# Optimization experiments

Measured on AMD Instinct MI355X. Metric: run time of the kernel, lower is better.

Reference implementation:

```python
import jax, jax.numpy as jnp
import numpy as np

B, T, F, H, D1, D2, OUT = 8192, 90, 7, 128, 128, 64, 30


def _layernorm(x, g, b, eps=1e-5):
    mu = jnp.mean(x, axis=-1, keepdims=True)
    var = jnp.mean((x - mu) ** 2, axis=-1, keepdims=True)
    return (x - mu) * jax.lax.rsqrt(var + eps) * g + b


def _lstm_layer(x, Wih, Whh, bih, bhh):
    # x: [B,T,H_in]; Wih: [4H,H_in]; Whh: [4H,H]; biases [4H]. PyTorch gate order i,f,g,o.
    xg = jnp.einsum('bti,gi->btg', x, Wih) + bih + bhh  # [B,T,4H] precomputed input projection
    xg_t = jnp.swapaxes(xg, 0, 1)  # [T,B,4H]

    def step(carry, gx):
        h, c = carry
        gates = gx + h @ Whh.T  # [B,4H]
        i, f, g, o = jnp.split(gates, 4, axis=-1)
        c = jax.nn.sigmoid(f) * c + jax.nn.sigmoid(i) * jnp.tanh(g)
        h = jax.nn.sigmoid(o) * jnp.tanh(c)
        return (h, c), h

    h0 = jnp.zeros((x.shape[0], H), x.dtype)
    (_, _), hs = jax.lax.scan(step, (h0, h0), xg_t)
    return jnp.swapaxes(hs, 0, 1)  # [B,T,H]


def setup_inputs() -> dict:
    key = jax.random.key(0)
    ks = jax.random.split(key, 16)
    s = lambda k, shape, scale: jax.random.normal(k, shape, jnp.float32) * scale
    inp = {
        'x': s(ks[0], (B, T, F), 1.0),
        'W_in': s(ks[1], (H, F), 0.3), 'b_in': jnp.zeros((H,)),
        'g_in': jnp.ones((H,)), 'be_in': jnp.zeros((H,)),
        'Wih0': s(ks[2], (4 * H, H), 0.08), 'Whh0': s(ks[3], (4 * H, H), 0.08),
        'bih0': jnp.zeros((4 * H,)).at[H:2 * H].set(1.0), 'bhh0': jnp.zeros((4 * H,)),
        'Wih1': s(ks[4], (4 * H, H), 0.08), 'Whh1': s(ks[5], (4 * H, H), 0.08),
        'bih1': jnp.zeros((4 * H,)).at[H:2 * H].set(1.0), 'bhh1': jnp.zeros((4 * H,)),
        'g_ln': jnp.ones((H,)), 'be_ln': jnp.zeros((H,)),
        'W_d1': s(ks[6], (D1, H), 0.12), 'b_d1': jnp.zeros((D1,)),
        'W_d2': s(ks[7], (D2, D1), 0.12), 'b_d2': jnp.zeros((D2,)),
        'W_d3': s(ks[8], (OUT, D2), 0.15), 'b_d3': jnp.zeros((OUT,)),
    }
    return inp


def reference(x, W_in, b_in, g_in, be_in,
              Wih0, Whh0, bih0, bhh0, Wih1, Whh1, bih1, bhh1,
              g_ln, be_ln, W_d1, b_d1, W_d2, b_d2, W_d3, b_d3):
    h = _layernorm(jnp.einsum('btf,hf->bth', x, W_in) + b_in, g_in, be_in)
    h = _lstm_layer(h, Wih0, Whh0, bih0, bhh0)
    h = _lstm_layer(h, Wih1, Whh1, bih1, bhh1)  # dropout between layers is eval no-op
    last = _layernorm(h[:, -1, :], g_ln, be_ln)  # [B,H]
    d = jax.nn.relu(last @ W_d1.T + b_d1)
    d = jax.nn.relu(d @ W_d2.T + b_d2)
    return d @ W_d3.T + b_d3  # [B,30]
```

## Files before the change

### kernel.cpp

```cpp
#include <hip/hip_runtime.h>

#define DEV __device__ __forceinline__
typedef unsigned short u16;
typedef unsigned int u32;
typedef __bf16 bf16x8 __attribute__((ext_vector_type(8)));
typedef float f32x4 __attribute__((ext_vector_type(4)));

static constexpr int B = 8192, T = 90, F = 7, H = 128, NOUT = 30;

DEV float fexp2(float x) { return __builtin_amdgcn_exp2f(x); }
DEV float frcp(float x) { return __builtin_amdgcn_rcpf(x); }
DEV float frsq(float x) { return __builtin_amdgcn_rsqf(x); }
DEV float sigm(float x) { return frcp(1.f + fexp2(-1.44269504088896341f * x)); }
DEV u16 f2bfbits(float f) { __bf16 b = (__bf16)f; return __builtin_bit_cast(u16, b); }
DEV float bfbits2f(u32 u) { return __builtin_bit_cast(float, u << 16); }
DEV u32 pk2(float a, float b) { return (u32)f2bfbits(a) | ((u32)f2bfbits(b) << 16); }

DEV float wave_sum(float v) {
#pragma unroll
    for (int m = 32; m; m >>= 1) v += __shfl_xor(v, m, 64);
    return v;
}

__global__ __launch_bounds__(512) void prep_aux(
    const float* __restrict__ W_in, const float* __restrict__ b_in,
    const float* __restrict__ g_in, const float* __restrict__ be_in,
    const float* __restrict__ Wih0, float* __restrict__ aux, u16* __restrict__ Uhat) {
    const int tid = threadIdx.x;
    if (tid < 7) {
        float sm = 0.f, sp = 0.f;
        for (int h = 0; h < 128; ++h) { const float w = W_in[h * 7 + tid]; sm += w; sp += w * b_in[h]; }
        aux[tid] = sm * (1.f / 128.f); aux[64 + tid] = sp * (1.f / 128.f);
    } else if (tid < 56) {
        const int cd = tid - 7, cc = cd / 7, dd = cd % 7;
        float s = 0.f;
        for (int h = 0; h < 128; ++h) s += W_in[h * 7 + cc] * W_in[h * 7 + dd];
        aux[8 + cd] = s * (1.f / 128.f);
    } else if (tid == 56) {
        float s = 0.f; for (int h = 0; h < 128; ++h) s += b_in[h];
        aux[7] = s * (1.f / 128.f);
    } else if (tid == 57) {
        float s = 0.f; for (int h = 0; h < 128; ++h) s += b_in[h] * b_in[h];
        aux[72] = s * (1.f / 128.f);
    }
    float acc[10];
#pragma unroll
    for (int i = 0; i < 10; ++i) acc[i] = 0.f;
    const float* wr = Wih0 + (long)tid * 128;
    for (int h = 0; h < 128; ++h) {
        const float wv = wr[h], wg = wv * g_in[h];
#pragma unroll
        for (int cc = 0; cc < 7; ++cc) acc[cc] += wg * W_in[h * 7 + cc];
        acc[7] += wg * b_in[h]; acc[8] += wg; acc[9] += wv * be_in[h];
    }
    u16* dst = Uhat + tid * 32;
#pragma unroll
    for (int cc = 0; cc < 10; ++cc) dst[cc] = f2bfbits(acc[cc]);
#pragma unroll
    for (int cc = 10; cc < 32; ++cc) dst[cc] = 0;
}

__global__ __launch_bounds__(256) void prep_stats(
    const float* __restrict__ x, const float* __restrict__ aux,
    float2* __restrict__ stats) {
    __shared__ float sa[80];
    const int tid = threadIdx.x;
    if (tid < 80) sa[tid] = aux[tid];
    __syncthreads();
    const long idx = (long)blockIdx.x * 256 + tid;
    const float* xr = x + idx * 7;
    float xv[7];
#pragma unroll
    for (int cc = 0; cc < 7; ++cc) xv[cc] = xr[cc];
    float mu = sa[7];
#pragma unroll
    for (int cc = 0; cc < 7; ++cc) mu += sa[cc] * xv[cc];
    float q = sa[72];
#pragma unroll
    for (int cc = 0; cc < 7; ++cc) {
        float tacc = 2.f * sa[64 + cc];
#pragma unroll
        for (int dd = 0; dd < 7; ++dd) tacc += sa[8 + cc * 7 + dd] * xv[dd];
        q += xv[cc] * tacc;
    }
    const float rstd = frsq(q - mu * mu + 1e-5f);
    stats[idx] = make_float2(rstd, -rstd * mu);
}

__global__ __launch_bounds__(512, 2) void lstm_rec_l1(
    const float* __restrict__ x, const float2* __restrict__ stats,
    const u16* __restrict__ Uhat, const float* __restrict__ Whh,
    const float* __restrict__ bih, const float* __restrict__ bhh,
    u16* __restrict__ hs) {
    __shared__ __align__(16) u16 s_z[2][2][4][16][8];
    __shared__ __align__(16) u16 s_h[2][2][16 * 128];

    const int tid = threadIdx.x;
    const int wave = tid >> 6, lane = tid & 63, quad = lane >> 4, n16 = lane & 15;
    const int b0 = blockIdx.x * 32;

    for (int i = tid; i < 2 * 2 * 4 * 16 * 8; i += 512) ((u16*)s_z)[i] = 0;
    for (int i = tid; i < 2 * 16 * 128; i += 512) ((u16*)s_h[1])[i] = 0;

    bf16x8 bU[4], bWhh[4][4];
    float bias[4];
#pragma unroll
    for (int g = 0; g < 4; ++g) {
        const int wrow = g * 128 + 16 * wave + n16;
        bias[g] = bih[wrow] + bhh[wrow];
        bU[g] = *(const bf16x8*)&Uhat[wrow * 32 + quad * 8];
#pragma unroll
        for (int kk = 0; kk < 4; ++kk) {
            const float* ph = Whh + (long)wrow * 128 + kk * 32 + quad * 8;
            bf16x8 bh;
#pragma unroll
            for (int j = 0; j < 8; ++j) bh[j] = (__bf16)ph[j];
            bWhh[g][kk] = bh;
        }
    }

    const f32x4 zero4 = {0.f, 0.f, 0.f, 0.f};
    float c[2][4];
#pragma unroll
    for (int mt = 0; mt < 2; ++mt)
#pragma unroll
        for (int r = 0; r < 4; ++r) c[mt][r] = 0.f;

    const bool stager = (lane < 8);
    const int tau = wave * 8 + lane;
    const int srow = tau & 31, skk8 = tau >> 5;
    const int smt = srow >> 4, sm = srow & 15;
    const long srowg = (long)(b0 + srow) * T;

    const int ftile = tid >> 8, finner = tid & 255;
    const int fm = finner & 15, fkk8 = finner >> 4;
    const int fldsoff = (fkk8 * 16 + fm) * 8;
    const size_t fgrow = (size_t)(b0 + ftile * 16 + fm) * T;
    const int fgcol = fkk8 * 8;

    __syncthreads();

    if (stager) {
        const float2 st0 = stats[srowg];
        u32 p0, p1, p2, p3;
        if (skk8 == 0) {
            const float* xp = x + srowg * 7;
            const float rs = st0.x;
            p0 = pk2(rs * xp[0], rs * xp[1]); p1 = pk2(rs * xp[2], rs * xp[3]);
            p2 = pk2(rs * xp[4], rs * xp[5]); p3 = pk2(rs * xp[6], rs);
        } else { p0 = pk2(st0.y, 1.f); p1 = 0; p2 = 0; p3 = 0; }
        *(uint4*)&s_z[0][smt][skk8][sm][0] = (uint4){p0, p1, p2, p3};
    }
    __syncthreads();

#pragma unroll 1
    for (int t = 0; t < T; ++t) {
        const int par = t & 1;
        const int t1 = t + 1;
        const bool hasPre = stager && (t1 < T);
        float2 nst = {};
        float nx[7];
        if (hasPre) {
            nst = stats[srowg + t1];
            if (skk8 == 0) {
                const float* xp = x + (srowg + t1) * 7;
#pragma unroll
                for (int j = 0; j < 7; ++j) nx[j] = xp[j];
            }
        }
        if (t > 0) {
            const uint4 hv = *(const uint4*)&s_h[par ^ 1][ftile][fldsoff];
            *(uint4*)(hs + (fgrow + (t - 1)) * 128 + fgcol) = hv;
        }

#pragma unroll
        for (int mt = 0; mt < 2; ++mt) {
            const bf16x8 az = *(const bf16x8*)&s_z[par][mt][quad][n16][0];
            bf16x8 ah[4];
#pragma unroll
            for (int kk = 0; kk < 4; ++kk)
                ah[kk] = *(const bf16x8*)&s_h[par ^ 1][mt][((kk * 4 + quad) * 16 + n16) * 8];
            f32x4 acc[4];
#pragma unroll
            for (int g = 0; g < 4; ++g) {
                f32x4 a = __builtin_amdgcn_mfma_f32_16x16x32_bf16(az, bU[g], zero4, 0, 0, 0);
#pragma unroll
                for (int kk = 0; kk < 4; ++kk)
                    a = __builtin_amdgcn_mfma_f32_16x16x32_bf16(ah[kk], bWhh[g][kk], a, 0, 0, 0);
                acc[g] = a;
            }
#pragma unroll
            for (int r = 0; r < 4; ++r) {
                const float xi = acc[0][r] + bias[0];
                const float xf = acc[1][r] + bias[1];
                const float xg = acc[2][r] + bias[2];
                const float xo = acc[3][r] + bias[3];
                const float tg = 2.f * frcp(1.f + fexp2(-2.88539008177792681f * xg)) - 1.f;
                const float cn = sigm(xf) * c[mt][r] + sigm(xi) * tg;
                c[mt][r] = cn;
                const float so = sigm(xo);
                const float rr = frcp(1.f + fexp2(-2.88539008177792681f * cn));
                const float hv = __builtin_fmaf(2.f * so, rr, -so);
                s_h[par][mt][((2 * wave + (n16 >> 3)) * 16 + (quad * 4 + r)) * 8 + (n16 & 7)] =
                    f2bfbits(hv);
            }
        }

        if (hasPre) {
            u32 p0, p1, p2, p3;
            if (skk8 == 0) {
                const float rs = nst.x;
                p0 = pk2(rs * nx[0], rs * nx[1]); p1 = pk2(rs * nx[2], rs * nx[3]);
                p2 = pk2(rs * nx[4], rs * nx[5]); p3 = pk2(rs * nx[6], rs);
            } else { p0 = pk2(nst.y, 1.f); p1 = 0; p2 = 0; p3 = 0; }
            *(uint4*)&s_z[par ^ 1][smt][skk8][sm][0] = (uint4){p0, p1, p2, p3};
        }
        __syncthreads();
    }
    {
        const uint4 hv = *(const uint4*)&s_h[1][ftile][fldsoff];
        *(uint4*)(hs + (fgrow + (T - 1)) * 128 + fgcol) = hv;
    }
}

__global__ __launch_bounds__(512, 2) void lstm_rec_l2(
    const float* __restrict__ Wih, const float* __restrict__ Whh,
    const float* __restrict__ bih, const float* __restrict__ bhh,
    const u16* __restrict__ xin, u16* __restrict__ hlast) {
    __shared__ __align__(16) u16 s_x[2][2][16 * 128];
    __shared__ __align__(16) u16 s_h[2][2][16 * 128];

    const int tid = threadIdx.x;
    const int wave = tid >> 6, lane = tid & 63, quad = lane >> 4, n16 = lane & 15;
    const int b0 = blockIdx.x * 32;

    for (int i = tid; i < 2 * 16 * 128; i += 512) ((u16*)s_h[1])[i] = 0;

    bf16x8 bWih[4][4], bWhh[4][4];
    float bias[4];
#pragma unroll
    for (int g = 0; g < 4; ++g) {
        const int wrow = g * 128 + 16 * wave + n16;
        bias[g] = bih[wrow] + bhh[wrow];
#pragma unroll
        for (int kk = 0; kk < 4; ++kk) {
            const float* pi = Wih + (long)wrow * 128 + kk * 32 + quad * 8;
            const float* ph = Whh + (long)wrow * 128 + kk * 32 + quad * 8;
            bf16x8 bi, bh;
#pragma unroll
            for (int j = 0; j < 8; ++j) { bi[j] = (__bf16)pi[j]; bh[j] = (__bf16)ph[j]; }
            bWih[g][kk] = bi; bWhh[g][kk] = bh;
        }
    }

    const f32x4 zero4 = {0.f, 0.f, 0.f, 0.f};
    float c[2][4];
#pragma unroll
    for (int mt = 0; mt < 2; ++mt)
#pragma unroll
        for (int r = 0; r < 4; ++r) c[mt][r] = 0.f;

    const int stile = tid >> 8, sinner = tid & 255;
    const int sm = sinner & 15, skk8 = sinner >> 4;
    const u16* gsrc = xin + (size_t)(b0 + stile * 16 + sm) * T * 128 + skk8 * 8;
    const int ftile = tid >> 8, finner = tid & 255;
    const int fm = finner & 15, fkk8 = finner >> 4;
    const int fldsoff = (fkk8 * 16 + fm) * 8;
    const int fgcol = fkk8 * 8;

    {
        const uint4 v = *(const uint4*)gsrc;
        *(uint4*)&s_x[0][stile][sinner * 8] = v;
    }
    __syncthreads();

#pragma unroll 1
    for (int t = 0; t < T; ++t) {
        const int par = t & 1;
        uint4 pre = {};
        const bool hasPre = (t + 1 < T);
        if (hasPre) pre = *(const uint4*)(gsrc + (size_t)(t + 1) * 128);

#pragma unroll
        for (int mt = 0; mt < 2; ++mt) {
            bf16x8 aln[4], ah[4];
#pragma unroll
            for (int kk = 0; kk < 4; ++kk) {
                aln[kk] = *(const bf16x8*)&s_x[par][mt][((kk * 4 + quad) * 16 + n16) * 8];
                ah[kk] = *(const bf16x8*)&s_h[par ^ 1][mt][((kk * 4 + quad) * 16 + n16) * 8];
            }
            f32x4 acc[4];
#pragma unroll
            for (int g = 0; g < 4; ++g) {
                f32x4 a = __builtin_amdgcn_mfma_f32_16x16x32_bf16(aln[0], bWih[g][0], zero4, 0, 0, 0);
                a = __builtin_amdgcn_mfma_f32_16x16x32_bf16(ah[0], bWhh[g][0], a, 0, 0, 0);
#pragma unroll
                for (int kk = 1; kk < 4; ++kk) {
                    a = __builtin_amdgcn_mfma_f32_16x16x32_bf16(aln[kk], bWih[g][kk], a, 0, 0, 0);
                    a = __builtin_amdgcn_mfma_f32_16x16x32_bf16(ah[kk], bWhh[g][kk], a, 0, 0, 0);
                }
                acc[g] = a;
            }
#pragma unroll
            for (int r = 0; r < 4; ++r) {
                const float xi = acc[0][r] + bias[0];
                const float xf = acc[1][r] + bias[1];
                const float xg = acc[2][r] + bias[2];
                const float xo = acc[3][r] + bias[3];
                const float tg = 2.f * frcp(1.f + fexp2(-2.88539008177792681f * xg)) - 1.f;
                const float cn = sigm(xf) * c[mt][r] + sigm(xi) * tg;
                c[mt][r] = cn;
                const float so = sigm(xo);
                const float rr = frcp(1.f + fexp2(-2.88539008177792681f * cn));
                const float hv = __builtin_fmaf(2.f * so, rr, -so);
                s_h[par][mt][((2 * wave + (n16 >> 3)) * 16 + (quad * 4 + r)) * 8 + (n16 & 7)] =
                    f2bfbits(hv);
            }
        }
        if (hasPre) *(uint4*)&s_x[par ^ 1][stile][sinner * 8] = pre;
        __syncthreads();
    }
    {
        const uint4 hv = *(const uint4*)&s_h[1][ftile][fldsoff];
        *(uint4*)(hlast + (size_t)(b0 + ftile * 16 + fm) * 128 + fgcol) = hv;
    }
}

__global__ __launch_bounds__(256) void dense_head(
    const u16* __restrict__ hlast, const float* __restrict__ g_ln,
    const float* __restrict__ be_ln, const float* __restrict__ W_d1,
    const float* __restrict__ b_d1, const float* __restrict__ W_d2,
    const float* __restrict__ b_d2, const float* __restrict__ W_d3,
    const float* __restrict__ b_d3, float* __restrict__ out) {
    __shared__ float s_ln[16][128];
    __shared__ float s_d1[16][128];
    __shared__ float s_d2[16][64];
    const int wave = threadIdx.x >> 6, lane = threadIdx.x & 63;
    const long base = (long)blockIdx.x * 16;
    const int R = wave * 4;

#pragma unroll
    for (int rr = 0; rr < 4; ++rr) {
        const long row = base + R + rr;
        const u32 packed = ((const u32*)hlast)[row * 64 + lane];
        float v0 = bfbits2f(packed & 0xffffu), v1 = bfbits2f(packed >> 16);
        const float s = wave_sum(v0 + v1);
        const float q = wave_sum(v0 * v0 + v1 * v1);
        const float mu = s * (1.f / 128.f);
        const float rstd = frsq(q * (1.f / 128.f) - mu * mu + 1e-5f);
        const int h0 = 2 * lane;
        s_ln[R + rr][h0] = (v0 - mu) * rstd * g_ln[h0] + be_ln[h0];
        s_ln[R + rr][h0 + 1] = (v1 - mu) * rstd * g_ln[h0 + 1] + be_ln[h0 + 1];
    }
    __syncthreads();

#pragma unroll
    for (int half = 0; half < 2; ++half) {
        const int o = lane + 64 * half;
        float a[4] = {b_d1[o], b_d1[o], b_d1[o], b_d1[o]};
        const float4* wr = (const float4*)(W_d1 + (long)o * 128);
#pragma unroll 8
        for (int k = 0; k < 32; ++k) {
            const float4 wv = wr[k];
#pragma unroll
            for (int rr = 0; rr < 4; ++rr) {
                const float4 xv = ((const float4*)s_ln[R + rr])[k];
                a[rr] += wv.x * xv.x + wv.y * xv.y + wv.z * xv.z + wv.w * xv.w;
            }
        }
#pragma unroll
        for (int rr = 0; rr < 4; ++rr) s_d1[R + rr][o] = fmaxf(a[rr], 0.f);
    }
    __syncthreads();

    {
        float a[4] = {b_d2[lane], b_d2[lane], b_d2[lane], b_d2[lane]};
        const float4* wr = (const float4*)(W_d2 + (long)lane * 128);
#pragma unroll 8
        for (int k = 0; k < 32; ++k) {
            const float4 wv = wr[k];
#pragma unroll
            for (int rr = 0; rr < 4; ++rr) {
                const float4 xv = ((const float4*)s_d1[R + rr])[k];
                a[rr] += wv.x * xv.x + wv.y * xv.y + wv.z * xv.z + wv.w * xv.w;
            }
        }
#pragma unroll
        for (int rr = 0; rr < 4; ++rr) s_d2[R + rr][lane] = fmaxf(a[rr], 0.f);
    }
    __syncthreads();

    if (lane < NOUT) {
        float a[4] = {b_d3[lane], b_d3[lane], b_d3[lane], b_d3[lane]};
        const float4* wr = (const float4*)(W_d3 + (long)lane * 64);
#pragma unroll
        for (int k = 0; k < 16; ++k) {
            const float4 wv = wr[k];
#pragma unroll
            for (int rr = 0; rr < 4; ++rr) {
                const float4 xv = ((const float4*)s_d2[R + rr])[k];
                a[rr] += wv.x * xv.x + wv.y * xv.y + wv.z * xv.z + wv.w * xv.w;
            }
        }
#pragma unroll
        for (int rr = 0; rr < 4; ++rr) out[(base + R + rr) * NOUT + lane] = a[rr];
    }
}

extern "C" void kernel_launch(void* const* d_in, const int* in_sizes, int n_in,
                              void* d_out, int out_size, void* d_ws, size_t ws_size,
                              hipStream_t stream) {
    const float* x = (const float*)d_in[0];
    const float* W_in = (const float*)d_in[1];
    const float* b_in = (const float*)d_in[2];
    const float* g_in = (const float*)d_in[3];
    const float* be_in = (const float*)d_in[4];
    const float* Wih0 = (const float*)d_in[5];
    const float* Whh0 = (const float*)d_in[6];
    const float* bih0 = (const float*)d_in[7];
    const float* bhh0 = (const float*)d_in[8];
    const float* Wih1 = (const float*)d_in[9];
    const float* Whh1 = (const float*)d_in[10];
    const float* bih1 = (const float*)d_in[11];
    const float* bhh1 = (const float*)d_in[12];
    const float* g_ln = (const float*)d_in[13];
    const float* be_ln = (const float*)d_in[14];
    const float* W_d1 = (const float*)d_in[15];
    const float* b_d1 = (const float*)d_in[16];
    const float* W_d2 = (const float*)d_in[17];
    const float* b_d2 = (const float*)d_in[18];
    const float* W_d3 = (const float*)d_in[19];
    const float* b_d3 = (const float*)d_in[20];
    float* out = (float*)d_out;

    char* w = (char*)d_ws;
    float* aux = (float*)w;               w += 512;
    u16* Uhat = (u16*)w;                  w += 512 * 32 * sizeof(u16);
    float2* stats = (float2*)w;           w += (size_t)B * T * sizeof(float2);
    u16* hs0 = (u16*)w;                   w += (size_t)B * T * H * sizeof(u16);
    u16* hlast = (u16*)w;

    prep_aux<<<1, 512, 0, stream>>>(W_in, b_in, g_in, be_in, Wih0, aux, Uhat);
    prep_stats<<<(B * T) / 256, 256, 0, stream>>>(x, aux, stats);
    lstm_rec_l1<<<B / 32, 512, 0, stream>>>(x, stats, Uhat, Whh0, bih0, bhh0, hs0);
    lstm_rec_l2<<<B / 32, 512, 0, stream>>>(Wih1, Whh1, bih1, bhh1, hs0, hlast);
    dense_head<<<B / 16, 256, 0, stream>>>(hlast, g_ln, be_ln, W_d1, b_d1, W_d2, b_d2,
                                           W_d3, b_d3, out);
}
```

Before: 552.9 us.

## Fuse both LSTM layers into one wavefront-pipelined kernel with split wave groups

Merges the two recurrent kernels into one launch. Four waves run layer 1 and four waves run layer 2 one timestep behind, passing h1 through shared memory. This removes the write and re-read of the full [B,T,H] layer-1 hidden sequence through global memory. In exchange each wave now holds twice as many weight fragments (two column tiles), which raises register pressure at 512 threads with occupancy 2. The layer-1 and layer-2 work per step also becomes unbalanced, and the waves meet at one barrier per step.

```diff
diff --git a/kernel.cpp b/kernel.cpp
--- a/kernel.cpp
+++ b/kernel.cpp
@@ -87,242 +87,216 @@
     stats[idx] = make_float2(rstd, -rstd * mu);
 }
 
-__global__ __launch_bounds__(512, 2) void lstm_rec_l1(
+#define GATE_E(ACC, CARR, PTR, HWB, R, B0, B1, B2, B3)                                  \
+    {                                                                                   \
+        const float xi_ = ACC[0][R] + (B0);                                             \
+        const float xf_ = ACC[1][R] + (B1);                                             \
+        const float xg_ = ACC[2][R] + (B2);                                             \
+        const float xo_ = ACC[3][R] + (B3);                                             \
+        const float tg_ = 2.f * frcp(1.f + fexp2(-2.88539008177792681f * xg_)) - 1.f;   \
+        const float cn_ = sigm(xf_) * CARR[R] + sigm(xi_) * tg_;                        \
+        CARR[R] = cn_;                                                                  \
+        const float so_ = sigm(xo_);                                                    \
+        const float rr_ = frcp(1.f + fexp2(-2.88539008177792681f * cn_));               \
+        (PTR)[(HWB) + (R) * 8] = f2bfbits(__builtin_fmaf(2.f * so_, rr_, -so_));        \
+    }
+
+__global__ __launch_bounds__(512, 2) void lstm_fused(
     const float* __restrict__ x, const float2* __restrict__ stats,
-    const u16* __restrict__ Uhat, const float* __restrict__ Whh,
-    const float* __restrict__ bih, const float* __restrict__ bhh,
-    u16* __restrict__ hs) {
+    const u16* __restrict__ Uhat,
+    const float* __restrict__ Whh0, const float* __restrict__ bih0,
+    const float* __restrict__ bhh0,
+    const float* __restrict__ Wih1, const float* __restrict__ Whh1,
+    const float* __restrict__ bih1, const float* __restrict__ bhh1,
+    u16* __restrict__ hlast) {
     __shared__ __align__(16) u16 s_z[2][2][4][16][8];
-    __shared__ __align__(16) u16 s_h[2][2][16 * 128];
+    __shared__ __align__(16) u16 s_h1[2][2][16][16][8];
+    __shared__ __align__(16) u16 s_h2[2][2][16][16][8];
 
     const int tid = threadIdx.x;
     const int wave = tid >> 6, lane = tid & 63, quad = lane >> 4, n16 = lane & 15;
     const int b0 = blockIdx.x * 32;
+    const int group = (wave ^ (wave >> 2)) & 1;
+    const int wl = wave >> 1;
 
     for (int i = tid; i < 2 * 2 * 4 * 16 * 8; i += 512) ((u16*)s_z)[i] = 0;
-    for (int i = tid; i < 2 * 16 * 128; i += 512) ((u16*)s_h[1])[i] = 0;
-
-    bf16x8 bU[4], bWhh[4][4];
-    float bias[4];
-#pragma unroll
-    for (int g = 0; g < 4; ++g) {
-        const int wrow = g * 128 + 16 * wave + n16;
-        bias[g] = bih[wrow] + bhh[wrow];
-        bU[g] = *(const bf16x8*)&Uhat[wrow * 32 + quad * 8];
-#pragma unroll
-        for (int kk = 0; kk < 4; ++kk) {
-            const float* ph = Whh + (long)wrow * 128 + kk * 32 + quad * 8;
-            bf16x8 bh;
-#pragma unroll
-            for (int j = 0; j < 8; ++j) bh[j] = (__bf16)ph[j];
-            bWhh[g][kk] = bh;
-        }
+    for (int i = tid; i < 2 * 16 * 16 * 8; i += 512) {
+        ((u16*)s_h1[1])[i] = 0;
+        ((u16*)s_h2[0])[i] = 0;
     }
 
     const f32x4 zero4 = {0.f, 0.f, 0.f, 0.f};
-    float c[2][4];
-#pragma unroll
-    for (int mt = 0; mt < 2; ++mt)
-#pragma unroll
-        for (int r = 0; r < 4; ++r) c[mt][r] = 0.f;
-
-    const bool stager = (lane < 8);
-    const int tau = wave * 8 + lane;
-    const int srow = tau & 31, skk8 = tau >> 5;
-    const int smt = srow >> 4, sm = srow & 15;
-    const long srowg = (long)(b0 + srow) * T;
-
-    const int ftile = tid >> 8, finner = tid & 255;
-    const int fm = finner & 15, fkk8 = finner >> 4;
-    const int fldsoff = (fkk8 * 16 + fm) * 8;
-    const size_t fgrow = (size_t)(b0 + ftile * 16 + fm) * T;
-    const int fgcol = fkk8 * 8;
+    const int hwb0 = ((wl * 4 + 0 + (n16 >> 3)) * 16 + quad * 4) * 8 + (n16 & 7);
+    const int hwb1 = ((wl * 4 + 2 + (n16 >> 3)) * 16 + quad * 4) * 8 + (n16 & 7);
 
     __syncthreads();
 
-    if (stager) {
-        const float2 st0 = stats[srowg];
-        u32 p0, p1, p2, p3;
-        if (skk8 == 0) {
+    if (group == 0) {
+        bf16x8 bU[4][2], bW0[4][2][4];
+        float bias[4][2];
+#pragma unroll
+        for (int g = 0; g < 4; ++g)
+#pragma unroll
+            for (int ct = 0; ct < 2; ++ct) {
+                const int wrow = g * 128 + wl * 32 + ct * 16 + n16;
+                bias[g][ct] = bih0[wrow] + bhh0[wrow];
+                bU[g][ct] = *(const bf16x8*)&Uhat[wrow * 32 + quad * 8];
+#pragma unroll
+                for (int kk = 0; kk < 4; ++kk) {
+                    const float* ph = Whh0 + (long)wrow * 128 + kk * 32 + quad * 8;
+                    bf16x8 bh;
+#pragma unroll
+                    for (int j = 0; j < 8; ++j) bh[j] = (__bf16)ph[j];
+                    bW0[g][ct][kk] = bh;
+                }
+            }
+
+        float c1[2][2][4];
+#pragma unroll
+        for (int mt = 0; mt < 2; ++mt)
+#pragma unroll
+            for (int ct = 0; ct < 2; ++ct)
+#pragma unroll
+                for (int r = 0; r < 4; ++r) c1[mt][ct][r] = 0.f;
+
+        const bool stager = (lane < 8);
+        const int srow = wl * 8 + lane, smt = srow >> 4, sm = srow & 15;
+        const long srowg = (long)(b0 + srow) * T;
+
+        if (stager) {
+            const float2 st0 = stats[srowg];
             const float* xp = x + srowg * 7;
             const float rs = st0.x;
-            p0 = pk2(rs * xp[0], rs * xp[1]); p1 = pk2(rs * xp[2], rs * xp[3]);
-            p2 = pk2(rs * xp[4], rs * xp[5]); p3 = pk2(rs * xp[6], rs);
-        } else { p0 = pk2(st0.y, 1.f); p1 = 0; p2 = 0; p3 = 0; }
-        *(uint4*)&s_z[0][smt][skk8][sm][0] = (uint4){p0, p1, p2, p3};
-    }
-    __syncthreads();
+            uint4 v0 = {pk2(rs * xp[0], rs * xp[1]), pk2(rs * xp[2], rs * xp[3]),
+                        pk2(rs * xp[4], rs * xp[5]), pk2(rs * xp[6], rs)};
+            uint4 v1 = {pk2(st0.y, 1.f), 0u, 0u, 0u};
+            *(uint4*)&s_z[0][smt][0][sm][0] = v0;
+            *(uint4*)&s_z[0][smt][1][sm][0] = v1;
+        }
+        __syncthreads();
 
 #pragma unroll 1
-    for (int t = 0; t < T; ++t) {
-        const int par = t & 1;
-        const int t1 = t + 1;
-        const bool hasPre = stager && (t1 < T);
-        float2 nst = {};
-        float nx[7];
-        if (hasPre) {
-            nst = stats[srowg + t1];
-            if (skk8 == 0) {
-                const float* xp = x + (srowg + t1) * 7;
-#pragma unroll
-                for (int j = 0; j < 7; ++j) nx[j] = xp[j];
-            }
-        }
-        if (t > 0) {
-            const uint4 hv = *(const uint4*)&s_h[par ^ 1][ftile][fldsoff];
-            *(uint4*)(hs + (fgrow + (t - 1)) * 128 + fgcol) = hv;
-        }
-
-#pragma unroll
-        for (int mt = 0; mt < 2; ++mt) {
-            const bf16x8 az = *(const bf16x8*)&s_z[par][mt][quad][n16][0];
-            bf16x8 ah[4];
-#pragma unroll
-            for (int kk = 0; kk < 4; ++kk)
-                ah[kk] = *(const bf16x8*)&s_h[par ^ 1][mt][((kk * 4 + quad) * 16 + n16) * 8];
-            f32x4 acc[4];
-#pragma unroll
-            for (int g = 0; g < 4; ++g) {
-                f32x4 a = __builtin_amdgcn_mfma_f32_16x16x32_bf16(az, bU[g], zero4, 0, 0, 0);
+        for (int k = 0; k < 90; ++k) {
+            const int par = k & 1;
+            float2 nst = {};
+            float nx0 = 0, nx1 = 0, nx2 = 0, nx3 = 0, nx4 = 0, nx5 = 0, nx6 = 0;
+            const bool pre = stager && (k < 89);
+            if (pre) {
+                nst = stats[srowg + k + 1];
+                const float* xp = x + (srowg + k + 1) * 7;
+                nx0 = xp[0]; nx1 = xp[1]; nx2 = xp[2]; nx3 = xp[3];
+                nx4 = xp[4]; nx5 = xp[5]; nx6 = xp[6];
+            }
+#pragma unroll
+            for (int mt = 0; mt < 2; ++mt) {
+                const bf16x8 az = *(const bf16x8*)&s_z[par][mt][quad][n16][0];
+                bf16x8 ah[4];
 #pragma unroll
                 for (int kk = 0; kk < 4; ++kk)
-                    a = __builtin_amdgcn_mfma_f32_16x16x32_bf16(ah[kk], bWhh[g][kk], a, 0, 0, 0);
-                acc[g] = a;
-            }
-#pragma unroll
-            for (int r = 0; r < 4; ++r) {
-                const float xi = acc[0][r] + bias[0];
-                const float xf = acc[1][r] + bias[1];
-                const float xg = acc[2][r] + bias[2];
-                const float xo = acc[3][r] + bias[3];
-                const float tg = 2.f * frcp(1.f + fexp2(-2.88539008177792681f * xg)) - 1.f;
-                const float cn = sigm(xf) * c[mt][r] + sigm(xi) * tg;
-                c[mt][r] = cn;
-                const float so = sigm(xo);
-                const float rr = frcp(1.f + fexp2(-2.88539008177792681f * cn));
-                const float hv = __builtin_fmaf(2.f * so, rr, -so);
-                s_h[par][mt][((2 * wave + (n16 >> 3)) * 16 + (quad * 4 + r)) * 8 + (n16 & 7)] =
-                    f2bfbits(hv);
-            }
-        }
-
-        if (hasPre) {
-            u32 p0, p1, p2, p3;
-            if (skk8 == 0) {
+                    ah[kk] = *(const bf16x8*)&s_h1[par ^ 1][mt][kk * 4 + quad][n16][0];
+                f32x4 acc[2][4];
+#pragma unroll
+                for (int ct = 0; ct < 2; ++ct)
+#pragma unroll
+                    for (int g = 0; g < 4; ++g) {
+                        f32x4 a = __builtin_amdgcn_mfma_f32_16x16x32_bf16(az, bU[g][ct], zero4, 0, 0, 0);
+#pragma unroll
+                        for (int kk = 0; kk < 4; ++kk)
+                            a = __builtin_amdgcn_mfma_f32_16x16x32_bf16(ah[kk], bW0[g][ct][kk], a, 0, 0, 0);
+                        acc[ct][g] = a;
+                    }
+                u16* hp = &s_h1[par][mt][0][0][0];
+#pragma unroll
+                for (int r = 0; r < 4; ++r)
+                    GATE_E(acc[0], c1[mt][0], hp, hwb0, r, bias[0][0], bias[1][0], bias[2][0], bias[3][0])
+#pragma unroll
+                for (int r = 0; r < 4; ++r)
+                    GATE_E(acc[1], c1[mt][1], hp, hwb1, r, bias[0][1], bias[1][1], bias[2][1], bias[3][1])
+            }
+            if (pre) {
                 const float rs = nst.x;
-                p0 = pk2(rs * nx[0], rs * nx[1]); p1 = pk2(rs * nx[2], rs * nx[3]);
-                p2 = pk2(rs * nx[4], rs * nx[5]); p3 = pk2(rs * nx[6], rs);
-            } else { p0 = pk2(nst.y, 1.f); p1 = 0; p2 = 0; p3 = 0; }
-            *(uint4*)&s_z[par ^ 1][smt][skk8][sm][0] = (uint4){p0, p1, p2, p3};
+                uint4 v0 = {pk2(rs * nx0, rs * nx1), pk2(rs * nx2, rs * nx3),
+                            pk2(rs * nx4, rs * nx5), pk2(rs * nx6, rs)};
+                uint4 v1 = {pk2(nst.y, 1.f), 0u, 0u, 0u};
+                *(uint4*)&s_z[par ^ 1][smt][0][sm][0] = v0;
+                *(uint4*)&s_z[par ^ 1][smt][1][sm][0] = v1;
+            }
+            __syncthreads();
         }
         __syncthreads();
-    }
+    } else {
+        bf16x8 bWi[4][2][4], bWh[4][2][4];
+        float bias[4][2];
+#pragma unroll
+        for (int g = 0; g < 4; ++g)
+#pragma unroll
+            for (int ct = 0; ct < 2; ++ct) {
+                const int wrow = g * 128 + wl * 32 + ct * 16 + n16;
+                bias[g][ct] = bih1[wrow] + bhh1[wrow];
+#pragma unroll
+                for (int kk = 0; kk < 4; ++kk) {
+                    const float* pi = Wih1 + (long)wrow * 128 + kk * 32 + quad * 8;
+                    const float* ph = Whh1 + (long)wrow * 128 + kk * 32 + quad * 8;
+                    bf16x8 bi, bh;
+#pragma unroll
+                    for (int j = 0; j < 8; ++j) { bi[j] = (__bf16)pi[j]; bh[j] = (__bf16)ph[j]; }
+                    bWi[g][ct][kk] = bi; bWh[g][ct][kk] = bh;
+                }
+            }
+
+        float c2[2][2][4];
+#pragma unroll
+        for (int mt = 0; mt < 2; ++mt)
+#pragma unroll
+            for (int ct = 0; ct < 2; ++ct)
+#pragma unroll
+                for (int r = 0; r < 4; ++r) c2[mt][ct][r] = 0.f;
+
+        __syncthreads();
+        __syncthreads();
+
+#pragma unroll 1
+        for (int k = 1; k <= 90; ++k) {
+            const int par = k & 1;
+#pragma unroll
+            for (int mt = 0; mt < 2; ++mt) {
+                bf16x8 a1[4], a2[4];
+#pragma unroll
+                for (int kk = 0; kk < 4; ++kk) {
+                    a1[kk] = *(const bf16x8*)&s_h1[par ^ 1][mt][kk * 4 + quad][n16][0];
+                    a2[kk] = *(const bf16x8*)&s_h2[par ^ 1][mt][kk * 4 + quad][n16][0];
+                }
+                f32x4 acc[2][4];
+#pragma unroll
+                for (int ct = 0; ct < 2; ++ct)
+#pragma unroll
+                    for (int g = 0; g < 4; ++g) {
+                        f32x4 a = __builtin_amdgcn_mfma_f32_16x16x32_bf16(a1[0], bWi[g][ct][0], zero4, 0, 0, 0);
+                        a = __builtin_amdgcn_mfma_f32_16x16x32_bf16(a2[0], bWh[g][ct][0], a, 0, 0, 0);
+#pragma unroll
+                        for (int kk = 1; kk < 4; ++kk) {
+                            a = __builtin_amdgcn_mfma_f32_16x16x32_bf16(a1[kk], bWi[g][ct][kk], a, 0, 0, 0);
+                            a = __builtin_amdgcn_mfma_f32_16x16x32_bf16(a2[kk], bWh[g][ct][kk], a, 0, 0, 0);
+                        }
+                        acc[ct][g] = a;
+                    }
+                u16* hp = &s_h2[par][mt][0][0][0];
+#pragma unroll
+                for (int r = 0; r < 4; ++r)
+                    GATE_E(acc[0], c2[mt][0], hp, hwb0, r, bias[0][0], bias[1][0], bias[2][0], bias[3][0])
+#pragma unroll
+                for (int r = 0; r < 4; ++r)
+                    GATE_E(acc[1], c2[mt][1], hp, hwb1, r, bias[0][1], bias[1][1], bias[2][1], bias[3][1])
+            }
+            __syncthreads();
+        }
+    }
+
     {
-        const uint4 hv = *(const uint4*)&s_h[1][ftile][fldsoff];
-        *(uint4*)(hs + (fgrow + (T - 1)) * 128 + fgcol) = hv;
-    }
-}
-
-__global__ __launch_bounds__(512, 2) void lstm_rec_l2(
-    const float* __restrict__ Wih, const float* __restrict__ Whh,
-    const float* __restrict__ bih, const float* __restrict__ bhh,
-    const u16* __restrict__ xin, u16* __restrict__ hlast) {
-    __shared__ __align__(16) u16 s_x[2][2][16 * 128];
-    __shared__ __align__(16) u16 s_h[2][2][16 * 128];
-
-    const int tid = threadIdx.x;
-    const int wave = tid >> 6, lane = tid & 63, quad = lane >> 4, n16 = lane & 15;
-    const int b0 = blockIdx.x * 32;
-
-    for (int i = tid; i < 2 * 16 * 128; i += 512) ((u16*)s_h[1])[i] = 0;
-
-    bf16x8 bWih[4][4], bWhh[4][4];
-    float bias[4];
-#pragma unroll
-    for (int g = 0; g < 4; ++g) {
-        const int wrow = g * 128 + 16 * wave + n16;
-        bias[g] = bih[wrow] + bhh[wrow];
-#pragma unroll
-        for (int kk = 0; kk < 4; ++kk) {
-            const float* pi = Wih + (long)wrow * 128 + kk * 32 + quad * 8;
-            const float* ph = Whh + (long)wrow * 128 + kk * 32 + quad * 8;
-            bf16x8 bi, bh;
-#pragma unroll
-            for (int j = 0; j < 8; ++j) { bi[j] = (__bf16)pi[j]; bh[j] = (__bf16)ph[j]; }
-            bWih[g][kk] = bi; bWhh[g][kk] = bh;
-        }
-    }
-
-    const f32x4 zero4 = {0.f, 0.f, 0.f, 0.f};
-    float c[2][4];
-#pragma unroll
-    for (int mt = 0; mt < 2; ++mt)
-#pragma unroll
-        for (int r = 0; r < 4; ++r) c[mt][r] = 0.f;
-
-    const int stile = tid >> 8, sinner = tid & 255;
-    const int sm = sinner & 15, skk8 = sinner >> 4;
-    const u16* gsrc = xin + (size_t)(b0 + stile * 16 + sm) * T * 128 + skk8 * 8;
-    const int ftile = tid >> 8, finner = tid & 255;
-    const int fm = finner & 15, fkk8 = finner >> 4;
-    const int fldsoff = (fkk8 * 16 + fm) * 8;
-    const int fgcol = fkk8 * 8;
-
-    {
-        const uint4 v = *(const uint4*)gsrc;
-        *(uint4*)&s_x[0][stile][sinner * 8] = v;
-    }
-    __syncthreads();
-
-#pragma unroll 1
-    for (int t = 0; t < T; ++t) {
-        const int par = t & 1;
-        uint4 pre = {};
-        const bool hasPre = (t + 1 < T);
-        if (hasPre) pre = *(const uint4*)(gsrc + (size_t)(t + 1) * 128);
-
-#pragma unroll
-        for (int mt = 0; mt < 2; ++mt) {
-            bf16x8 aln[4], ah[4];
-#pragma unroll
-            for (int kk = 0; kk < 4; ++kk) {
-                aln[kk] = *(const bf16x8*)&s_x[par][mt][((kk * 4 + quad) * 16 + n16) * 8];
-                ah[kk] = *(const bf16x8*)&s_h[par ^ 1][mt][((kk * 4 + quad) * 16 + n16) * 8];
-            }
-            f32x4 acc[4];
-#pragma unroll
-            for (int g = 0; g < 4; ++g) {
-                f32x4 a = __builtin_amdgcn_mfma_f32_16x16x32_bf16(aln[0], bWih[g][0], zero4, 0, 0, 0);
-                a = __builtin_amdgcn_mfma_f32_16x16x32_bf16(ah[0], bWhh[g][0], a, 0, 0, 0);
-#pragma unroll
-                for (int kk = 1; kk < 4; ++kk) {
-                    a = __builtin_amdgcn_mfma_f32_16x16x32_bf16(aln[kk], bWih[g][kk], a, 0, 0, 0);
-                    a = __builtin_amdgcn_mfma_f32_16x16x32_bf16(ah[kk], bWhh[g][kk], a, 0, 0, 0);
-                }
-                acc[g] = a;
-            }
-#pragma unroll
-            for (int r = 0; r < 4; ++r) {
-                const float xi = acc[0][r] + bias[0];
-                const float xf = acc[1][r] + bias[1];
-                const float xg = acc[2][r] + bias[2];
-                const float xo = acc[3][r] + bias[3];
-                const float tg = 2.f * frcp(1.f + fexp2(-2.88539008177792681f * xg)) - 1.f;
-                const float cn = sigm(xf) * c[mt][r] + sigm(xi) * tg;
-                c[mt][r] = cn;
-                const float so = sigm(xo);
-                const float rr = frcp(1.f + fexp2(-2.88539008177792681f * cn));
-                const float hv = __builtin_fmaf(2.f * so, rr, -so);
-                s_h[par][mt][((2 * wave + (n16 >> 3)) * 16 + (quad * 4 + r)) * 8 + (n16 & 7)] =
-                    f2bfbits(hv);
-            }
-        }
-        if (hasPre) *(uint4*)&s_x[par ^ 1][stile][sinner * 8] = pre;
-        __syncthreads();
-    }
-    {
-        const uint4 hv = *(const uint4*)&s_h[1][ftile][fldsoff];
-        *(uint4*)(hlast + (size_t)(b0 + ftile * 16 + fm) * 128 + fgcol) = hv;
+        const int ftile = tid >> 8, fin = tid & 255;
+        const int fm = fin & 15, fk = fin >> 4;
+        const uint4 hv = *(const uint4*)&s_h2[0][ftile][fk][fm][0];
+        *(uint4*)(hlast + (size_t)(b0 + ftile * 16 + fm) * 128 + fk * 8) = hv;
     }
 }
 
@@ -437,13 +411,12 @@
     float* aux = (float*)w;               w += 512;
     u16* Uhat = (u16*)w;                  w += 512 * 32 * sizeof(u16);
     float2* stats = (float2*)w;           w += (size_t)B * T * sizeof(float2);
-    u16* hs0 = (u16*)w;                   w += (size_t)B * T * H * sizeof(u16);
     u16* hlast = (u16*)w;
 
     prep_aux<<<1, 512, 0, stream>>>(W_in, b_in, g_in, be_in, Wih0, aux, Uhat);
     prep_stats<<<(B * T) / 256, 256, 0, stream>>>(x, aux, stats);
-    lstm_rec_l1<<<B / 32, 512, 0, stream>>>(x, stats, Uhat, Whh0, bih0, bhh0, hs0);
-    lstm_rec_l2<<<B / 32, 512, 0, stream>>>(Wih1, Whh1, bih1, bhh1, hs0, hlast);
+    lstm_fused<<<B / 32, 512, 0, stream>>>(x, stats, Uhat, Whh0, bih0, bhh0,
+                                           Wih1, Whh1, bih1, bhh1, hlast);
     dense_head<<<B / 16, 256, 0, stream>>>(hlast, g_ln, be_ln, W_d1, b_d1, W_d2, b_d2,
                                            W_d3, b_d3, out);
 }
```

After: 1.499 ms. +171.1%, slower.

## Halve LSTM block batch tile to 16 rows to double grid size

Applied to the files above, without the earlier changes.

Both recurrent LSTM kernels now process 16 batch rows per block instead of 32, launching B/16 blocks. Each wave runs one M-tile of MFMAs per timestep instead of two, which shortens the serial per-step critical path and exposes more blocks to fill the CUs. The cost is that each block still loads the full weight set into registers, so weight loads are duplicated across twice as many blocks. Half the threads now sit idle during staging and stores, and per-step work is smaller relative to the barrier overhead.

```diff
diff --git a/kernel.cpp b/kernel.cpp
--- a/kernel.cpp
+++ b/kernel.cpp
@@ -87,20 +87,34 @@
     stats[idx] = make_float2(rstd, -rstd * mu);
 }
 
+#define GATE_R(ACC, CARR, SHROW, R)                                                     \
+    {                                                                                   \
+        const float xi_ = ACC[0][R] + bias[0];                                          \
+        const float xf_ = ACC[1][R] + bias[1];                                          \
+        const float xg_ = ACC[2][R] + bias[2];                                          \
+        const float xo_ = ACC[3][R] + bias[3];                                          \
+        const float tg_ = 2.f * frcp(1.f + fexp2(-2.88539008177792681f * xg_)) - 1.f;   \
+        const float cn_ = sigm(xf_) * CARR[R] + sigm(xi_) * tg_;                        \
+        CARR[R] = cn_;                                                                  \
+        const float so_ = sigm(xo_);                                                    \
+        const float rr_ = frcp(1.f + fexp2(-2.88539008177792681f * cn_));               \
+        SHROW[hwbase + (R) * 8] = f2bfbits(__builtin_fmaf(2.f * so_, rr_, -so_));       \
+    }
+
 __global__ __launch_bounds__(512, 2) void lstm_rec_l1(
     const float* __restrict__ x, const float2* __restrict__ stats,
     const u16* __restrict__ Uhat, const float* __restrict__ Whh,
     const float* __restrict__ bih, const float* __restrict__ bhh,
     u16* __restrict__ hs) {
-    __shared__ __align__(16) u16 s_z[2][2][4][16][8];
-    __shared__ __align__(16) u16 s_h[2][2][16 * 128];
+    __shared__ __align__(16) u16 s_z[2][4][16][8];
+    __shared__ __align__(16) u16 s_h[2][16 * 128];
 
     const int tid = threadIdx.x;
     const int wave = tid >> 6, lane = tid & 63, quad = lane >> 4, n16 = lane & 15;
-    const int b0 = blockIdx.x * 32;
-
-    for (int i = tid; i < 2 * 2 * 4 * 16 * 8; i += 512) ((u16*)s_z)[i] = 0;
-    for (int i = tid; i < 2 * 16 * 128; i += 512) ((u16*)s_h[1])[i] = 0;
+    const int b0 = blockIdx.x * 16;
+
+    for (int i = tid; i < 2 * 4 * 16 * 8; i += 512) ((u16*)s_z)[i] = 0;
+    for (int i = tid; i < 16 * 128; i += 512) s_h[1][i] = 0;
 
     bf16x8 bU[4], bWhh[4][4];
     float bias[4];
@@ -120,23 +134,21 @@
     }
 
     const f32x4 zero4 = {0.f, 0.f, 0.f, 0.f};
-    float c[2][4];
-#pragma unroll
-    for (int mt = 0; mt < 2; ++mt)
-#pragma unroll
-        for (int r = 0; r < 4; ++r) c[mt][r] = 0.f;
-
-    const bool stager = (lane < 8);
-    const int tau = wave * 8 + lane;
-    const int srow = tau & 31, skk8 = tau >> 5;
-    const int smt = srow >> 4, sm = srow & 15;
+    float c[4];
+#pragma unroll
+    for (int r = 0; r < 4; ++r) c[r] = 0.f;
+
+    const bool stager = (lane < 4);
+    const int tau = wave * 4 + lane;
+    const int srow = tau & 15, skk8 = tau >> 4;
     const long srowg = (long)(b0 + srow) * T;
 
-    const int ftile = tid >> 8, finner = tid & 255;
-    const int fm = finner & 15, fkk8 = finner >> 4;
+    const int fm = tid & 15, fkk8 = (tid >> 4) & 15;
     const int fldsoff = (fkk8 * 16 + fm) * 8;
-    const size_t fgrow = (size_t)(b0 + ftile * 16 + fm) * T;
+    const size_t fgrow = (size_t)(b0 + fm) * T;
     const int fgcol = fkk8 * 8;
+
+    const int hwbase = (2 * wave + (n16 >> 3)) * 128 + quad * 32 + (n16 & 7);
 
     __syncthreads();
 
@@ -149,61 +161,49 @@
             p0 = pk2(rs * xp[0], rs * xp[1]); p1 = pk2(rs * xp[2], rs * xp[3]);
             p2 = pk2(rs * xp[4], rs * xp[5]); p3 = pk2(rs * xp[6], rs);
         } else { p0 = pk2(st0.y, 1.f); p1 = 0; p2 = 0; p3 = 0; }
-        *(uint4*)&s_z[0][smt][skk8][sm][0] = (uint4){p0, p1, p2, p3};
+        *(uint4*)&s_z[0][skk8][srow][0] = (uint4){p0, p1, p2, p3};
     }
     __syncthreads();
 
 #pragma unroll 1
     for (int t = 0; t < T; ++t) {
         const int par = t & 1;
-        const int t1 = t + 1;
-        const bool hasPre = stager && (t1 < T);
+        const bool hasPre = stager && (t + 1 < T);
         float2 nst = {};
         float nx[7];
         if (hasPre) {
-            nst = stats[srowg + t1];
+            nst = stats[srowg + t + 1];
             if (skk8 == 0) {
-                const float* xp = x + (srowg + t1) * 7;
+                const float* xp = x + (srowg + t + 1) * 7;
 #pragma unroll
                 for (int j = 0; j < 7; ++j) nx[j] = xp[j];
             }
         }
-        if (t > 0) {
-            const uint4 hv = *(const uint4*)&s_h[par ^ 1][ftile][fldsoff];
+        if (t > 0 && tid < 256) {
+            const uint4 hv = *(const uint4*)&s_h[par ^ 1][fldsoff];
             *(uint4*)(hs + (fgrow + (t - 1)) * 128 + fgcol) = hv;
         }
 
-#pragma unroll
-        for (int mt = 0; mt < 2; ++mt) {
-            const bf16x8 az = *(const bf16x8*)&s_z[par][mt][quad][n16][0];
-            bf16x8 ah[4];
+        const bf16x8 az = *(const bf16x8*)&s_z[par][quad][n16][0];
+        bf16x8 ah[4];
+#pragma unroll
+        for (int kk = 0; kk < 4; ++kk)
+            ah[kk] = *(const bf16x8*)&s_h[par ^ 1][((kk * 4 + quad) * 16 + n16) * 8];
+        f32x4 acc[4];
+#pragma unroll
+        for (int g = 0; g < 4; ++g) {
+            f32x4 a = __builtin_amdgcn_mfma_f32_16x16x32_bf16(az, bU[g], zero4, 0, 0, 0);
 #pragma unroll
             for (int kk = 0; kk < 4; ++kk)
-                ah[kk] = *(const bf16x8*)&s_h[par ^ 1][mt][((kk * 4 + quad) * 16 + n16) * 8];
-            f32x4 acc[4];
-#pragma unroll
-            for (int g = 0; g < 4; ++g) {
-                f32x4 a = __builtin_amdgcn_mfma_f32_16x16x32_bf16(az, bU[g], zero4, 0, 0, 0);
-#pragma unroll
-                for (int kk = 0; kk < 4; ++kk)
-                    a = __builtin_amdgcn_mfma_f32_16x16x32_bf16(ah[kk], bWhh[g][kk], a, 0, 0, 0);
-                acc[g] = a;
-            }
-#pragma unroll
-            for (int r = 0; r < 4; ++r) {
-                const float xi = acc[0][r] + bias[0];
-                const float xf = acc[1][r] + bias[1];
-                const float xg = acc[2][r] + bias[2];
-                const float xo = acc[3][r] + bias[3];
-                const float tg = 2.f * frcp(1.f + fexp2(-2.88539008177792681f * xg)) - 1.f;
-                const float cn = sigm(xf) * c[mt][r] + sigm(xi) * tg;
-                c[mt][r] = cn;
-                const float so = sigm(xo);
-                const float rr = frcp(1.f + fexp2(-2.88539008177792681f * cn));
-                const float hv = __builtin_fmaf(2.f * so, rr, -so);
-                s_h[par][mt][((2 * wave + (n16 >> 3)) * 16 + (quad * 4 + r)) * 8 + (n16 & 7)] =
-                    f2bfbits(hv);
-            }
+                a = __builtin_amdgcn_mfma_f32_16x16x32_bf16(ah[kk], bWhh[g][kk], a, 0, 0, 0);
+            acc[g] = a;
+        }
+        {
+            u16* hp = s_h[par];
+            GATE_R(acc, c, hp, 0)
+            GATE_R(acc, c, hp, 1)
+            GATE_R(acc, c, hp, 2)
+            GATE_R(acc, c, hp, 3)
         }
 
         if (hasPre) {
@@ -213,12 +213,12 @@
                 p0 = pk2(rs * nx[0], rs * nx[1]); p1 = pk2(rs * nx[2], rs * nx[3]);
                 p2 = pk2(rs * nx[4], rs * nx[5]); p3 = pk2(rs * nx[6], rs);
             } else { p0 = pk2(nst.y, 1.f); p1 = 0; p2 = 0; p3 = 0; }
-            *(uint4*)&s_z[par ^ 1][smt][skk8][sm][0] = (uint4){p0, p1, p2, p3};
+            *(uint4*)&s_z[par ^ 1][skk8][srow][0] = (uint4){p0, p1, p2, p3};
         }
         __syncthreads();
     }
-    {
-        const uint4 hv = *(const uint4*)&s_h[1][ftile][fldsoff];
+    if (tid < 256) {
+        const uint4 hv = *(const uint4*)&s_h[1][fldsoff];
         *(uint4*)(hs + (fgrow + (T - 1)) * 128 + fgcol) = hv;
     }
 }
@@ -227,14 +227,14 @@
     const float* __restrict__ Wih, const float* __restrict__ Whh,
     const float* __restrict__ bih, const float* __restrict__ bhh,
     const u16* __restrict__ xin, u16* __restrict__ hlast) {
-    __shared__ __align__(16) u16 s_x[2][2][16 * 128];
-    __shared__ __align__(16) u16 s_h[2][2][16 * 128];
+    __shared__ __align__(16) u16 s_x[2][16 * 128];
+    __shared__ __align__(16) u16 s_h[2][16 * 128];
 
     const int tid = threadIdx.x;
     const int wave = tid >> 6, lane = tid & 63, quad = lane >> 4, n16 = lane & 15;
-    const int b0 = blockIdx.x * 32;
-
-    for (int i = tid; i < 2 * 16 * 128; i += 512) ((u16*)s_h[1])[i] = 0;
+    const int b0 = blockIdx.x * 16;
+
+    for (int i = tid; i < 16 * 128; i += 512) s_h[1][i] = 0;
 
     bf16x8 bWih[4][4], bWhh[4][4];
     float bias[4];
@@ -254,23 +254,19 @@
     }
 
     const f32x4 zero4 = {0.f, 0.f, 0.f, 0.f};
-    float c[2][4];
-#pragma unroll
-    for (int mt = 0; mt < 2; ++mt)
-#pragma unroll
-        for (int r = 0; r < 4; ++r) c[mt][r] = 0.f;
-
-    const int stile = tid >> 8, sinner = tid & 255;
-    const int sm = sinner & 15, skk8 = sinner >> 4;
-    const u16* gsrc = xin + (size_t)(b0 + stile * 16 + sm) * T * 128 + skk8 * 8;
-    const int ftile = tid >> 8, finner = tid & 255;
-    const int fm = finner & 15, fkk8 = finner >> 4;
-    const int fldsoff = (fkk8 * 16 + fm) * 8;
-    const int fgcol = fkk8 * 8;
-
-    {
+    float c[4];
+#pragma unroll
+    for (int r = 0; r < 4; ++r) c[r] = 0.f;
+
+    const int ssm = tid & 15, sskk8 = (tid >> 4) & 15;
+    const u16* gsrc = xin + (size_t)(b0 + ssm) * T * 128 + sskk8 * 8;
+    const int soff = (sskk8 * 16 + ssm) * 8;
+
+    const int hwbase = (2 * wave + (n16 >> 3)) * 128 + quad * 32 + (n16 & 7);
+
+    if (tid < 256) {
         const uint4 v = *(const uint4*)gsrc;
-        *(uint4*)&s_x[0][stile][sinner * 8] = v;
+        *(uint4*)&s_x[0][soff] = v;
     }
     __syncthreads();
 
@@ -278,51 +274,41 @@
     for (int t = 0; t < T; ++t) {
         const int par = t & 1;
         uint4 pre = {};
-        const bool hasPre = (t + 1 < T);
+        const bool hasPre = (t + 1 < T) && (tid < 256);
         if (hasPre) pre = *(const uint4*)(gsrc + (size_t)(t + 1) * 128);
 
-#pragma unroll
-        for (int mt = 0; mt < 2; ++mt) {
-            bf16x8 aln[4], ah[4];
-#pragma unroll
-            for (int kk = 0; kk < 4; ++kk) {
-                aln[kk] = *(const bf16x8*)&s_x[par][mt][((kk * 4 + quad) * 16 + n16) * 8];
-                ah[kk] = *(const bf16x8*)&s_h[par ^ 1][mt][((kk * 4 + quad) * 16 + n16) * 8];
+        bf16x8 aln[4], ah[4];
+#pragma unroll
+        for (int kk = 0; kk < 4; ++kk) {
+            const int ro = ((kk * 4 + quad) * 16 + n16) * 8;
+            aln[kk] = *(const bf16x8*)&s_x[par][ro];
+            ah[kk] = *(const bf16x8*)&s_h[par ^ 1][ro];
+        }
+        f32x4 acc[4];
+#pragma unroll
+        for (int g = 0; g < 4; ++g) {
+            f32x4 a = __builtin_amdgcn_mfma_f32_16x16x32_bf16(aln[0], bWih[g][0], zero4, 0, 0, 0);
+            a = __builtin_amdgcn_mfma_f32_16x16x32_bf16(ah[0], bWhh[g][0], a, 0, 0, 0);
+#pragma unroll
+            for (int kk = 1; kk < 4; ++kk) {
+                a = __builtin_amdgcn_mfma_f32_16x16x32_bf16(aln[kk], bWih[g][kk], a, 0, 0, 0);
+                a = __builtin_amdgcn_mfma_f32_16x16x32_bf16(ah[kk], bWhh[g][kk], a, 0, 0, 0);
             }
-            f32x4 acc[4];
-#pragma unroll
-            for (int g = 0; g < 4; ++g) {
-                f32x4 a = __builtin_amdgcn_mfma_f32_16x16x32_bf16(aln[0], bWih[g][0], zero4, 0, 0, 0);
-                a = __builtin_amdgcn_mfma_f32_16x16x32_bf16(ah[0], bWhh[g][0], a, 0, 0, 0);
-#pragma unroll
-                for (int kk = 1; kk < 4; ++kk) {
-                    a = __builtin_amdgcn_mfma_f32_16x16x32_bf16(aln[kk], bWih[g][kk], a, 0, 0, 0);
-                    a = __builtin_amdgcn_mfma_f32_16x16x32_bf16(ah[kk], bWhh[g][kk], a, 0, 0, 0);
-                }
-                acc[g] = a;
-            }
-#pragma unroll
-            for (int r = 0; r < 4; ++r) {
-                const float xi = acc[0][r] + bias[0];
-                const float xf = acc[1][r] + bias[1];
-                const float xg = acc[2][r] + bias[2];
-                const float xo = acc[3][r] + bias[3];
-                const float tg = 2.f * frcp(1.f + fexp2(-2.88539008177792681f * xg)) - 1.f;
-                const float cn = sigm(xf) * c[mt][r] + sigm(xi) * tg;
-                c[mt][r] = cn;
-                const float so = sigm(xo);
-                const float rr = frcp(1.f + fexp2(-2.88539008177792681f * cn));
-                const float hv = __builtin_fmaf(2.f * so, rr, -so);
-                s_h[par][mt][((2 * wave + (n16 >> 3)) * 16 + (quad * 4 + r)) * 8 + (n16 & 7)] =
-                    f2bfbits(hv);
-            }
-        }
-        if (hasPre) *(uint4*)&s_x[par ^ 1][stile][sinner * 8] = pre;
+            acc[g] = a;
+        }
+        {
+            u16* hp = s_h[par];
+            GATE_R(acc, c, hp, 0)
+            GATE_R(acc, c, hp, 1)
+            GATE_R(acc, c, hp, 2)
+            GATE_R(acc, c, hp, 3)
+        }
+        if (hasPre) *(uint4*)&s_x[par ^ 1][soff] = pre;
         __syncthreads();
     }
-    {
-        const uint4 hv = *(const uint4*)&s_h[1][ftile][fldsoff];
-        *(uint4*)(hlast + (size_t)(b0 + ftile * 16 + fm) * 128 + fgcol) = hv;
+    if (tid < 256) {
+        const uint4 hv = *(const uint4*)&s_h[1][soff];
+        *(uint4*)(hlast + (size_t)(b0 + ssm) * 128 + sskk8 * 8) = hv;
     }
 }
 
@@ -442,8 +428,8 @@
 
     prep_aux<<<1, 512, 0, stream>>>(W_in, b_in, g_in, be_in, Wih0, aux, Uhat);
     prep_stats<<<(B * T) / 256, 256, 0, stream>>>(x, aux, stats);
-    lstm_rec_l1<<<B / 32, 512, 0, stream>>>(x, stats, Uhat, Whh0, bih0, bhh0, hs0);
-    lstm_rec_l2<<<B / 32, 512, 0, stream>>>(Wih1, Whh1, bih1, bhh1, hs0, hlast);
+    lstm_rec_l1<<<B / 16, 512, 0, stream>>>(x, stats, Uhat, Whh0, bih0, bhh0, hs0);
+    lstm_rec_l2<<<B / 16, 512, 0, stream>>>(Wih1, Whh1, bih1, bhh1, hs0, hlast);
     dense_head<<<B / 16, 256, 0, stream>>>(hlast, g_ln, be_ln, W_d1, b_d1, W_d2, b_d2,
                                            W_d3, b_d3, out);
 }
```

Result: slower. 644.7 us (+16.6%).
